# Kernel optimization log

Hardware: AMD Instinct MI355X
Metric: run time of the kernel (lower is better)

## Reference

```python
import jax, jax.numpy as jnp
import numpy as np

DIM = 192
HEADS = 6
WS = 7        # window_size
SS = 3        # shift_size
MLP_RATIO = 4.0
B = 64
H_RES = 56
W_RES = 56
EPS = 1e-5


def _rel_index(ws):
    # standard Swin relative position index, (ws*ws, ws*ws) int
    coords = np.stack(np.meshgrid(np.arange(ws), np.arange(ws), indexing='ij'))  # 2,ws,ws
    flat = coords.reshape(2, -1)                                                 # 2,N
    rel = (flat[:, :, None] - flat[:, None, :]).transpose(1, 2, 0)               # N,N,2
    rel[:, :, 0] += ws - 1
    rel[:, :, 1] += ws - 1
    rel[:, :, 0] *= 2 * ws - 1
    return rel.sum(-1)  # N,N


def _attn_mask(H, W, ws, ss):
    # (num_windows, N, N) float mask with 0 / -100, static given H,W,ws,ss
    img = np.zeros((H, W))
    sl = (slice(0, -ws), slice(-ws, -ss), slice(-ss, None))
    cnt = 0
    for hs in sl:
        for wsl in sl:
            img[hs, wsl] = cnt
            cnt += 1
    mw = img.reshape(H // ws, ws, W // ws, ws).transpose(0, 2, 1, 3).reshape(-1, ws * ws)
    diff = mw[:, None, :] - mw[:, :, None]
    return jnp.asarray(np.where(diff != 0, -100.0, 0.0).astype(np.float32))


def _ln(x, g, b):
    mu = x.mean(-1, keepdims=True)
    var = jnp.var(x, axis=-1, keepdims=True)
    return (x - mu) * jax.lax.rsqrt(var + EPS) * g + b


def setup_inputs() -> dict:
    key = jax.random.key(0)
    ks = jax.random.split(key, 8)
    C = DIM
    hid = int(C * MLP_RATIO)
    nrm = lambda k, s: jax.random.normal(k, s, jnp.float32) * 0.02
    return {
        "x": jax.random.normal(ks[0], (B, H_RES * W_RES, C), jnp.float32),
        "norm1_g": jnp.ones((C,), jnp.float32),
        "norm1_b": jnp.zeros((C,), jnp.float32),
        "qkv_w": nrm(ks[1], (3 * C, C)),
        "qkv_b": jnp.zeros((3 * C,), jnp.float32),
        "rel_bias_table": nrm(ks[2], ((2 * WS - 1) ** 2, HEADS)),
        "proj_w": nrm(ks[3], (C, C)),
        "proj_b": jnp.zeros((C,), jnp.float32),
        "norm2_g": jnp.ones((C,), jnp.float32),
        "norm2_b": jnp.zeros((C,), jnp.float32),
        "fc1_w": nrm(ks[4], (hid, C)),
        "fc1_b": jnp.zeros((hid,), jnp.float32),
        "fc2_w": nrm(ks[5], (C, hid)),
        "fc2_b": jnp.zeros((C,), jnp.float32),
        "H": H_RES,
        "W": W_RES,
    }


def _block(x, norm1_g, norm1_b, qkv_w, qkv_b, rel_bias_table, proj_w, proj_b,
           norm2_g, norm2_b, fc1_w, fc1_b, fc2_w, fc2_b, H, W):
    Bn, L, C = x.shape
    ws = min(WS, H, W)
    ss = SS if ws > SS else 0
    nH, nW = H // ws, W // ws
    N = ws * ws
    hd = C // HEADS

    shortcut = x
    h = _ln(x, norm1_g, norm1_b).reshape(Bn, H, W, C)
    if ss > 0:
        h = jnp.roll(h, (-ss, -ss), axis=(1, 2))
    # window partition -> (Bn*nH*nW, N, C)
    win = h.reshape(Bn, nH, ws, nW, ws, C).transpose(0, 1, 3, 2, 4, 5).reshape(-1, N, C)

    qkv = win @ qkv_w.T + qkv_b                       # (nWin, N, 3C)
    qkv = qkv.reshape(-1, N, 3, HEADS, hd).transpose(2, 0, 3, 1, 4)
    q, k, v = qkv[0], qkv[1], qkv[2]                  # (nWin, heads, N, hd)
    scale = float(hd) ** -0.5
    attn = jnp.einsum('whnd,whmd->whnm', q * scale, k)

    idx = _rel_index(ws)                              # N,N (static)
    bias = rel_bias_table[idx.reshape(-1)].reshape(N, N, HEADS).transpose(2, 0, 1)
    attn = attn + bias[None]

    if ss > 0:
        mask = _attn_mask(H, W, ws, ss)               # (nH*nW, N, N)
        attn = attn.reshape(Bn, nH * nW, HEADS, N, N) + mask[None, :, None]
        attn = attn.reshape(-1, HEADS, N, N)

    attn = jax.nn.softmax(attn, axis=-1)
    out = jnp.einsum('whnm,whmd->whnd', attn, v)      # (nWin, heads, N, hd)
    out = out.transpose(0, 2, 1, 3).reshape(-1, N, C)
    out = out @ proj_w.T + proj_b

    # window reverse -> (Bn, H, W, C)
    out = out.reshape(Bn, nH, nW, ws, ws, C).transpose(0, 1, 3, 2, 4, 5).reshape(Bn, H, W, C)
    if ss > 0:
        out = jnp.roll(out, (ss, ss), axis=(1, 2))
    x = shortcut + out.reshape(Bn, H * W, C)

    h2 = _ln(x, norm2_g, norm2_b)
    h2 = jax.nn.gelu(h2 @ fc1_w.T + fc1_b, approximate=False)
    h2 = h2 @ fc2_w.T + fc2_b
    return x + h2


def reference(x, norm1_g, norm1_b, qkv_w, qkv_b, rel_bias_table, proj_w, proj_b,
              norm2_g, norm2_b, fc1_w, fc1_b, fc2_w, fc2_b, H, W):
    return _block(x, norm1_g, norm1_b, qkv_w, qkv_b, rel_bias_table, proj_w, proj_b,
                  norm2_g, norm2_b, fc1_w, fc1_b, fc2_w, fc2_b, H, W)
```

## Files before the change

### kernel.cpp

```cpp
#include <hip/hip_runtime.h>
#include <math.h>

typedef __attribute__((ext_vector_type(8))) short short8;
typedef __attribute__((ext_vector_type(4))) float floatx4;
typedef __attribute__((ext_vector_type(4))) float fvec4;

__device__ __forceinline__ float bf2f(unsigned short u) {
    union { unsigned int i; float f; } v;
    v.i = ((unsigned int)u) << 16;
    return v.f;
}
__device__ __forceinline__ unsigned short f2bf(float f) {
    union { float f; unsigned int i; } v;
    v.f = f;
    return (unsigned short)((v.i + 0x7FFFu + ((v.i >> 16) & 1u)) >> 16);
}
__device__ __forceinline__ void async16(const void* g, void* l) {
    __builtin_amdgcn_global_load_lds((const __attribute__((address_space(1))) void*)g,
                                     (__attribute__((address_space(3))) void*)l, 16, 0, 0);
}
__device__ __forceinline__ int region(int c) { return c < 49 ? 0 : (c < 53 ? 1 : 2); }

__global__ __launch_bounds__(256) void cvt_kernel(const float* __restrict__ s,
                                                  unsigned short* __restrict__ d, int n) {
    int i = blockIdx.x * 256 + threadIdx.x;
    if (i < n) d[i] = f2bf(s[i]);
}

__global__ __launch_bounds__(256) void ln_kernel(const float* __restrict__ src,
                                                 const float* __restrict__ gw,
                                                 const float* __restrict__ bw,
                                                 unsigned short* __restrict__ dst,
                                                 int mode) {
    int o = blockIdx.x * 4 + (threadIdx.x >> 6);
    int lane = threadIdx.x & 63;
    size_t srow;
    if (mode == 0) {
        int win = o / 49, n = o % 49;
        int b = win >> 6, wl = win & 63;
        int wh = wl >> 3, ww = wl & 7;
        int i = n / 7, j = n % 7;
        int pr = (wh * 7 + i + 3) % 56;
        int pc = (ww * 7 + j + 3) % 56;
        srow = ((size_t)b * 3136 + (size_t)(pr * 56 + pc)) * 192;
    } else {
        srow = (size_t)o * 192;
    }
    float v0 = src[srow + lane];
    float v1 = src[srow + lane + 64];
    float v2 = src[srow + lane + 128];
    float s = v0 + v1 + v2;
    float s2 = v0 * v0 + v1 * v1 + v2 * v2;
    #pragma unroll
    for (int off = 32; off > 0; off >>= 1) {
        s += __shfl_xor(s, off);
        s2 += __shfl_xor(s2, off);
    }
    float mean = s * (1.0f / 192.0f);
    float var = s2 * (1.0f / 192.0f) - mean * mean;
    float inv = rsqrtf(var + 1e-5f);
    size_t drow = (size_t)o * 192;
    dst[drow + lane]       = f2bf((v0 - mean) * inv * gw[lane]       + bw[lane]);
    dst[drow + lane + 64]  = f2bf((v1 - mean) * inv * gw[lane + 64]  + bw[lane + 64]);
    dst[drow + lane + 128] = f2bf((v2 - mean) * inv * gw[lane + 128] + bw[lane + 128]);
}

template <int EPI>
__global__ __launch_bounds__(256) void gemm_nt(const unsigned short* __restrict__ A,
                                               const unsigned short* __restrict__ W,
                                               const float* __restrict__ bias,
                                               int K, int ldo, int mbase,
                                               unsigned short* __restrict__ outb,
                                               float* __restrict__ outf,
                                               const float* __restrict__ resid) {
    __shared__ __align__(16) unsigned short Al[128][32];
    __shared__ __align__(16) unsigned short Wl[64][32];
    int tid = threadIdx.x;
    int lane = tid & 63;
    int wv = tid >> 6;
    int wm = wv >> 1, wn = wv & 1;
    int m0 = blockIdx.y * 128;
    int n0 = blockIdx.x * 64;
    int quad = lane >> 4, l15 = lane & 15;

    int srow = lane >> 2;
    int scol = (lane & 3) * 8;
    const unsigned short* aP0 = A + (size_t)(m0 + wv * 32 + srow) * K + scol;
    const unsigned short* aP1 = aP0 + (size_t)16 * K;
    const unsigned short* wP  = W + (size_t)(n0 + wv * 16 + srow) * K + scol;
    unsigned short* lA0 = &Al[wv * 32][0];
    unsigned short* lA1 = &Al[wv * 32 + 16][0];
    unsigned short* lW  = &Wl[wv * 16][0];

    floatx4 acc[4][2];
    floatx4 zero = {0.f, 0.f, 0.f, 0.f};
    #pragma unroll
    for (int a = 0; a < 4; ++a)
        #pragma unroll
        for (int b = 0; b < 2; ++b) acc[a][b] = zero;

    for (int kt = 0; kt < K; kt += 32) {
        __syncthreads();
        async16(aP0 + kt, lA0);
        async16(aP1 + kt, lA1);
        async16(wP + kt, lW);
        __syncthreads();
        short8 af[4], wf[2];
        #pragma unroll
        for (int mt = 0; mt < 4; ++mt)
            af[mt] = *(const short8*)&Al[wm * 64 + mt * 16 + l15][quad * 8];
        #pragma unroll
        for (int nt = 0; nt < 2; ++nt)
            wf[nt] = *(const short8*)&Wl[wn * 32 + nt * 16 + l15][quad * 8];
        #pragma unroll
        for (int mt = 0; mt < 4; ++mt)
            #pragma unroll
            for (int nt = 0; nt < 2; ++nt)
                acc[mt][nt] = __builtin_amdgcn_mfma_f32_16x16x32_bf16(af[mt], wf[nt], acc[mt][nt], 0, 0, 0);
    }

    #pragma unroll
    for (int mt = 0; mt < 4; ++mt) {
        #pragma unroll
        for (int nt = 0; nt < 2; ++nt) {
            #pragma unroll
            for (int r = 0; r < 4; ++r) {
                int m = m0 + wm * 64 + mt * 16 + quad * 4 + r;
                int n = n0 + wn * 32 + nt * 16 + l15;
                float v = acc[mt][nt][r] + bias[n];
                if (EPI == 0) {
                    outb[(size_t)m * ldo + n] = f2bf(v);
                } else if (EPI == 1) {
                    float g = 0.5f * v * (1.0f + erff(v * 0.70710678118654752f));
                    outb[(size_t)m * ldo + n] = f2bf(g);
                } else if (EPI == 2) {
                    int win = m / 49, np = m % 49;
                    int b = win >> 6, wl = win & 63;
                    int wh = wl >> 3, ww = wl & 7;
                    int i = np / 7, j = np % 7;
                    int pr = (wh * 7 + i + 3) % 56;
                    int pc = (ww * 7 + j + 3) % 56;
                    size_t dst = ((size_t)b * 3136 + (size_t)(pr * 56 + pc)) * 192 + n;
                    outf[dst] = resid[dst] + v;
                } else {
                    size_t dst = (size_t)(mbase + m) * ldo + n;
                    outf[dst] = resid[dst] + v;
                }
            }
        }
    }
}

__global__ __launch_bounds__(192) void attn_kernel(const unsigned short* __restrict__ qkv,
                                                   const float* __restrict__ btab,
                                                   unsigned short* __restrict__ awin) {
    __shared__ __align__(16) unsigned short VT[3][32][72];
    __shared__ __align__(16) unsigned short Pb[3][64][72];
    __shared__ float bl[1014];
    int w = blockIdx.x >> 1;
    int hb = (blockIdx.x & 1) * 3;
    int tid = threadIdx.x;
    int hl = tid >> 6;
    int lane = tid & 63;
    int h = hb + hl;
    int quad = lane >> 4, l15 = lane & 15;
    const unsigned short* base = qkv + (size_t)w * 49 * 576;

    for (int i = tid; i < 1014; i += 192) bl[i] = btab[i];
    for (int idx = lane; idx < 512; idx += 64) {
        VT[hl][idx >> 4][48 + (idx & 15)] = 0;
    }
    for (int idx = lane; idx < 196; idx += 64) {
        int r = idx >> 2, c8 = (idx & 3) * 8;
        short8 vv = *(const short8*)(base + (size_t)r * 576 + 384 + h * 32 + c8);
        #pragma unroll
        for (int e = 0; e < 8; ++e) VT[hl][c8 + e][r] = (unsigned short)vv[e];
    }
    short8 qf[4], kf[4];
    #pragma unroll
    for (int mt = 0; mt < 4; ++mt)
        qf[mt] = *(const short8*)(base + (size_t)(mt * 16 + l15) * 576 + h * 32 + quad * 8);
    #pragma unroll
    for (int nt = 0; nt < 4; ++nt)
        kf[nt] = *(const short8*)(base + (size_t)(nt * 16 + l15) * 576 + 192 + h * 32 + quad * 8);

    floatx4 zero = {0.f, 0.f, 0.f, 0.f};
    floatx4 S[4][4];
    #pragma unroll
    for (int mt = 0; mt < 4; ++mt)
        #pragma unroll
        for (int nt = 0; nt < 4; ++nt)
            S[mt][nt] = __builtin_amdgcn_mfma_f32_16x16x32_bf16(qf[mt], kf[nt], zero, 0, 0, 0);

    __syncthreads();

    int wl = w & 63, wh7 = (wl >> 3) * 7, ww7 = (wl & 7) * 7;
    int coli[4], colj[4], colrid[4], colok[4];
    #pragma unroll
    for (int nt = 0; nt < 4; ++nt) {
        int c = nt * 16 + l15;
        colok[nt] = c < 49;
        int ci = c / 7;
        coli[nt] = ci;
        colj[nt] = c - ci * 7;
        colrid[nt] = region(wh7 + ci) * 3 + region(ww7 + (c - ci * 7));
    }
    const float scale = 0.17677669529663687f;
    float rinv[4][4];
    #pragma unroll
    for (int mt = 0; mt < 4; ++mt) {
        #pragma unroll
        for (int rr = 0; rr < 4; ++rr) {
            int r = mt * 16 + quad * 4 + rr;
            int ri = r / 7, rj = r - ri * 7;
            int rowrid = region(wh7 + ri) * 3 + region(ww7 + rj);
            float vv[4];
            float mx = -3.0e38f;
            #pragma unroll
            for (int nt = 0; nt < 4; ++nt) {
                float v;
                if (colok[nt]) {
                    v = S[mt][nt][rr] * scale +
                        bl[((ri - coli[nt] + 6) * 13 + (rj - colj[nt] + 6)) * 6 + h];
                    if (colrid[nt] != rowrid) v -= 100.f;
                } else {
                    v = -3.0e38f;
                }
                vv[nt] = v;
                mx = fmaxf(mx, v);
            }
            #pragma unroll
            for (int s = 1; s <= 8; s <<= 1) mx = fmaxf(mx, __shfl_xor(mx, s));
            float sum = 0.f;
            #pragma unroll
            for (int nt = 0; nt < 4; ++nt) {
                float e = __expf(vv[nt] - mx);
                vv[nt] = e;
                sum += e;
            }
            #pragma unroll
            for (int s = 1; s <= 8; s <<= 1) sum += __shfl_xor(sum, s);
            rinv[mt][rr] = 1.f / sum;
            #pragma unroll
            for (int nt = 0; nt < 4; ++nt) Pb[hl][r][nt * 16 + l15] = f2bf(vv[nt]);
        }
    }

    floatx4 O[4][2];
    #pragma unroll
    for (int mt = 0; mt < 4; ++mt)
        #pragma unroll
        for (int nt = 0; nt < 2; ++nt) O[mt][nt] = zero;
    #pragma unroll
    for (int ks = 0; ks < 2; ++ks) {
        short8 vf[2];
        #pragma unroll
        for (int nt = 0; nt < 2; ++nt)
            vf[nt] = *(const short8*)&VT[hl][nt * 16 + l15][ks * 32 + quad * 8];
        #pragma unroll
        for (int mt = 0; mt < 4; ++mt) {
            short8 pf = *(const short8*)&Pb[hl][mt * 16 + l15][ks * 32 + quad * 8];
            #pragma unroll
            for (int nt = 0; nt < 2; ++nt)
                O[mt][nt] = __builtin_amdgcn_mfma_f32_16x16x32_bf16(pf, vf[nt], O[mt][nt], 0, 0, 0);
        }
    }
    #pragma unroll
    for (int mt = 0; mt < 4; ++mt) {
        #pragma unroll
        for (int rr = 0; rr < 4; ++rr) {
            int r = mt * 16 + quad * 4 + rr;
            if (r < 49) {
                float inv = rinv[mt][rr];
                #pragma unroll
                for (int nt = 0; nt < 2; ++nt)
                    awin[((size_t)w * 49 + r) * 192 + h * 32 + nt * 16 + l15] =
                        f2bf(O[mt][nt][rr] * inv);
            }
        }
    }
}

extern "C" void kernel_launch(void* const* d_in, const int* in_sizes, int n_in,
                              void* d_out, int out_size, void* d_ws, size_t ws_size,
                              hipStream_t stream) {
    const float* x      = (const float*)d_in[0];
    const float* n1g    = (const float*)d_in[1];
    const float* n1b    = (const float*)d_in[2];
    const float* qkv_w  = (const float*)d_in[3];
    const float* qkv_b  = (const float*)d_in[4];
    const float* btab   = (const float*)d_in[5];
    const float* proj_w = (const float*)d_in[6];
    const float* proj_b = (const float*)d_in[7];
    const float* n2g    = (const float*)d_in[8];
    const float* n2b    = (const float*)d_in[9];
    const float* fc1_w  = (const float*)d_in[10];
    const float* fc1_b  = (const float*)d_in[11];
    const float* fc2_w  = (const float*)d_in[12];
    const float* fc2_b  = (const float*)d_in[13];
    float* out = (float*)d_out;

    char* p = (char*)d_ws;
    size_t off = 0;
    auto alloc = [&](size_t bytes) {
        char* r = p + off;
        off = (off + bytes + 255) & ~(size_t)255;
        return r;
    };
    unsigned short* wq   = (unsigned short*)alloc((size_t)576 * 192 * 2);
    unsigned short* wp   = (unsigned short*)alloc((size_t)192 * 192 * 2);
    unsigned short* w1   = (unsigned short*)alloc((size_t)768 * 192 * 2);
    unsigned short* w2   = (unsigned short*)alloc((size_t)192 * 768 * 2);
    unsigned short* hwin = (unsigned short*)alloc((size_t)200704 * 192 * 2);
    unsigned short* qkvb = (unsigned short*)alloc((size_t)200704 * 576 * 2);
    float*          xres = (float*)alloc((size_t)200704 * 192 * 4);
    unsigned short* g1   = (unsigned short*)alloc((size_t)50176 * 768 * 2);
    if (ws_size < off) return;

    cvt_kernel<<<432, 256, 0, stream>>>(qkv_w, wq, 110592);
    cvt_kernel<<<144, 256, 0, stream>>>(proj_w, wp, 36864);
    cvt_kernel<<<576, 256, 0, stream>>>(fc1_w, w1, 147456);
    cvt_kernel<<<576, 256, 0, stream>>>(fc2_w, w2, 147456);

    ln_kernel<<<50176, 256, 0, stream>>>(x, n1g, n1b, hwin, 0);
    gemm_nt<0><<<dim3(9, 1568), 256, 0, stream>>>(hwin, wq, qkv_b, 192, 576, 0, qkvb, nullptr, nullptr);
    attn_kernel<<<8192, 192, 0, stream>>>(qkvb, btab, hwin );
    gemm_nt<2><<<dim3(3, 1568), 256, 0, stream>>>(hwin, wp, proj_b, 192, 192, 0, nullptr, xres, x);
    unsigned short* h2 = qkvb;
    ln_kernel<<<50176, 256, 0, stream>>>(xres, n2g, n2b, h2, 1);
    for (int c = 0; c < 4; ++c) {
        int mb = c * 50176;
        gemm_nt<1><<<dim3(12, 392), 256, 0, stream>>>(h2 + (size_t)mb * 192, w1, fc1_b, 192, 768, 0,
                                                      g1, nullptr, nullptr);
        gemm_nt<3><<<dim3(3, 392), 256, 0, stream>>>(g1, w2, fc2_b, 768, 192, mb,
                                                     nullptr, out, xres);
    }
}
```

Baseline: 1.133 ms.

## Precompute bias+mask table as MFMA accumulator init and simplify attention softmax

Folds the attention scale into the Q rows of the QKV weights and bias during conversion. A 4-class × heads table of relative bias plus shift mask is precomputed and fed as the MFMA accumulator init. Scores are computed transposed so the per-query sum needs only two cross-lane shuffles. The max subtraction and the LDS transpose of V are dropped, so V is gathered straight from global memory and the block barrier goes away. This removes per-element index math, shared-memory bias loads and sync, at the cost of strided 2-byte V loads and no overflow guard in the exponent.

```diff
diff --git a/kernel.cpp b/kernel.cpp
--- a/kernel.cpp
+++ b/kernel.cpp
@@ -1,9 +1,9 @@
 #include <hip/hip_runtime.h>
+#include <hip/hip_bf16.h>
 #include <math.h>
 
 typedef __attribute__((ext_vector_type(8))) short short8;
 typedef __attribute__((ext_vector_type(4))) float floatx4;
-typedef __attribute__((ext_vector_type(4))) float fvec4;
 
 __device__ __forceinline__ float bf2f(unsigned short u) {
     union { unsigned int i; float f; } v;
@@ -19,12 +19,39 @@
     __builtin_amdgcn_global_load_lds((const __attribute__((address_space(1))) void*)g,
                                      (__attribute__((address_space(3))) void*)l, 16, 0, 0);
 }
-__device__ __forceinline__ int region(int c) { return c < 49 ? 0 : (c < 53 ? 1 : 2); }
 
 __global__ __launch_bounds__(256) void cvt_kernel(const float* __restrict__ s,
-                                                  unsigned short* __restrict__ d, int n) {
+                                                  unsigned short* __restrict__ d, int n,
+                                                  int cut, float scale) {
     int i = blockIdx.x * 256 + threadIdx.x;
-    if (i < n) d[i] = f2bf(s[i]);
+    if (i < n) d[i] = f2bf(s[i] * (i < cut ? scale : 1.0f));
+}
+__global__ __launch_bounds__(256) void biasscale_kernel(const float* __restrict__ s,
+                                                        float* __restrict__ d, int n,
+                                                        int cut, float scale) {
+    int i = blockIdx.x * 256 + threadIdx.x;
+    if (i < n) d[i] = s[i] * (i < cut ? scale : 1.0f);
+}
+
+__global__ __launch_bounds__(256) void bmt_kernel(const float* __restrict__ btab,
+                                                  float* __restrict__ tbl) {
+    int idx = blockIdx.x * 256 + threadIdx.x;
+    int key = idx & 63;
+    int q = (idx >> 6) & 63;
+    int h = (idx >> 12) % 6;
+    int cls = idx / (4096 * 6);
+    float v;
+    if (key >= 49) v = -3.0e38f;
+    else if (q >= 49) v = 0.0f;
+    else {
+        int qi = q / 7, qj = q % 7, ki = key / 7, kj = key % 7;
+        v = btab[((qi - ki + 6) * 13 + (qj - kj + 6)) * 6 + h];
+        int whT = (cls >> 1) & 1, wwT = cls & 1;
+        int rq = (whT ? (qi < 4 ? 1 : 2) : 0) * 3 + (wwT ? (qj < 4 ? 1 : 2) : 0);
+        int rk = (whT ? (ki < 4 ? 1 : 2) : 0) * 3 + (wwT ? (kj < 4 ? 1 : 2) : 0);
+        if (rq != rk) v -= 100.0f;
+    }
+    tbl[idx] = v;
 }
 
 __global__ __launch_bounds__(256) void ln_kernel(const float* __restrict__ src,
@@ -152,101 +179,74 @@
 }
 
 __global__ __launch_bounds__(192) void attn_kernel(const unsigned short* __restrict__ qkv,
-                                                   const float* __restrict__ btab,
+                                                   const float* __restrict__ tbl,
                                                    unsigned short* __restrict__ awin) {
-    __shared__ __align__(16) unsigned short VT[3][32][72];
     __shared__ __align__(16) unsigned short Pb[3][64][72];
-    __shared__ float bl[1014];
     int w = blockIdx.x >> 1;
     int hb = (blockIdx.x & 1) * 3;
-    int tid = threadIdx.x;
-    int hl = tid >> 6;
-    int lane = tid & 63;
+    int hl = threadIdx.x >> 6;
     int h = hb + hl;
+    int lane = threadIdx.x & 63;
     int quad = lane >> 4, l15 = lane & 15;
     const unsigned short* base = qkv + (size_t)w * 49 * 576;
-
-    for (int i = tid; i < 1014; i += 192) bl[i] = btab[i];
-    for (int idx = lane; idx < 512; idx += 64) {
-        VT[hl][idx >> 4][48 + (idx & 15)] = 0;
-    }
-    for (int idx = lane; idx < 196; idx += 64) {
-        int r = idx >> 2, c8 = (idx & 3) * 8;
-        short8 vv = *(const short8*)(base + (size_t)r * 576 + 384 + h * 32 + c8);
-        #pragma unroll
-        for (int e = 0; e < 8; ++e) VT[hl][c8 + e][r] = (unsigned short)vv[e];
-    }
-    short8 qf[4], kf[4];
+    int wl = w & 63;
+    int cls = ((wl >> 3) == 7 ? 2 : 0) + ((wl & 7) == 7 ? 1 : 0);
+    const float* tb = tbl + (size_t)(cls * 6 + h) * 4096;
+
+    short8 kf[4], qf[4];
     #pragma unroll
     for (int mt = 0; mt < 4; ++mt)
-        qf[mt] = *(const short8*)(base + (size_t)(mt * 16 + l15) * 576 + h * 32 + quad * 8);
+        kf[mt] = *(const short8*)(base + (size_t)(mt * 16 + l15) * 576 + 192 + h * 32 + quad * 8);
     #pragma unroll
     for (int nt = 0; nt < 4; ++nt)
-        kf[nt] = *(const short8*)(base + (size_t)(nt * 16 + l15) * 576 + 192 + h * 32 + quad * 8);
-
+        qf[nt] = *(const short8*)(base + (size_t)(nt * 16 + l15) * 576 + h * 32 + quad * 8);
+
+    floatx4 S[4][4];
+    #pragma unroll
+    for (int mt = 0; mt < 4; ++mt)
+        #pragma unroll
+        for (int nt = 0; nt < 4; ++nt) {
+            floatx4 cinit = *(const floatx4*)(tb + (nt * 16 + l15) * 64 + mt * 16 + quad * 4);
+            S[mt][nt] = __builtin_amdgcn_mfma_f32_16x16x32_bf16(kf[mt], qf[nt], cinit, 0, 0, 0);
+        }
+
+    #pragma unroll
+    for (int mt = 0; mt < 4; ++mt)
+        #pragma unroll
+        for (int nt = 0; nt < 4; ++nt)
+            #pragma unroll
+            for (int rr = 0; rr < 4; ++rr)
+                S[mt][nt][rr] = __expf(S[mt][nt][rr]);
+
+    float rinv[4];
+    #pragma unroll
+    for (int nt = 0; nt < 4; ++nt) {
+        float s = 0.f;
+        #pragma unroll
+        for (int mt = 0; mt < 4; ++mt)
+            s += (S[mt][nt][0] + S[mt][nt][1]) + (S[mt][nt][2] + S[mt][nt][3]);
+        s += __shfl_xor(s, 16);
+        s += __shfl_xor(s, 32);
+        rinv[nt] = 1.0f / s;
+    }
+
+    #pragma unroll
+    for (int mt = 0; mt < 4; ++mt) {
+        #pragma unroll
+        for (int nt = 0; nt < 4; ++nt) {
+            __hip_bfloat162 p0 = __float22bfloat162_rn(
+                make_float2(S[mt][nt][0] * rinv[nt], S[mt][nt][1] * rinv[nt]));
+            __hip_bfloat162 p1 = __float22bfloat162_rn(
+                make_float2(S[mt][nt][2] * rinv[nt], S[mt][nt][3] * rinv[nt]));
+            union { __hip_bfloat162 h2[2]; uint2 u; } pk;
+            pk.h2[0] = p0;
+            pk.h2[1] = p1;
+            *(uint2*)&Pb[hl][nt * 16 + l15][mt * 16 + quad * 4] = pk.u;
+        }
+    }
+
+    floatx4 O[4][2];
     floatx4 zero = {0.f, 0.f, 0.f, 0.f};
-    floatx4 S[4][4];
-    #pragma unroll
-    for (int mt = 0; mt < 4; ++mt)
-        #pragma unroll
-        for (int nt = 0; nt < 4; ++nt)
-            S[mt][nt] = __builtin_amdgcn_mfma_f32_16x16x32_bf16(qf[mt], kf[nt], zero, 0, 0, 0);
-
-    __syncthreads();
-
-    int wl = w & 63, wh7 = (wl >> 3) * 7, ww7 = (wl & 7) * 7;
-    int coli[4], colj[4], colrid[4], colok[4];
-    #pragma unroll
-    for (int nt = 0; nt < 4; ++nt) {
-        int c = nt * 16 + l15;
-        colok[nt] = c < 49;
-        int ci = c / 7;
-        coli[nt] = ci;
-        colj[nt] = c - ci * 7;
-        colrid[nt] = region(wh7 + ci) * 3 + region(ww7 + (c - ci * 7));
-    }
-    const float scale = 0.17677669529663687f;
-    float rinv[4][4];
-    #pragma unroll
-    for (int mt = 0; mt < 4; ++mt) {
-        #pragma unroll
-        for (int rr = 0; rr < 4; ++rr) {
-            int r = mt * 16 + quad * 4 + rr;
-            int ri = r / 7, rj = r - ri * 7;
-            int rowrid = region(wh7 + ri) * 3 + region(ww7 + rj);
-            float vv[4];
-            float mx = -3.0e38f;
-            #pragma unroll
-            for (int nt = 0; nt < 4; ++nt) {
-                float v;
-                if (colok[nt]) {
-                    v = S[mt][nt][rr] * scale +
-                        bl[((ri - coli[nt] + 6) * 13 + (rj - colj[nt] + 6)) * 6 + h];
-                    if (colrid[nt] != rowrid) v -= 100.f;
-                } else {
-                    v = -3.0e38f;
-                }
-                vv[nt] = v;
-                mx = fmaxf(mx, v);
-            }
-            #pragma unroll
-            for (int s = 1; s <= 8; s <<= 1) mx = fmaxf(mx, __shfl_xor(mx, s));
-            float sum = 0.f;
-            #pragma unroll
-            for (int nt = 0; nt < 4; ++nt) {
-                float e = __expf(vv[nt] - mx);
-                vv[nt] = e;
-                sum += e;
-            }
-            #pragma unroll
-            for (int s = 1; s <= 8; s <<= 1) sum += __shfl_xor(sum, s);
-            rinv[mt][rr] = 1.f / sum;
-            #pragma unroll
-            for (int nt = 0; nt < 4; ++nt) Pb[hl][r][nt * 16 + l15] = f2bf(vv[nt]);
-        }
-    }
-
-    floatx4 O[4][2];
     #pragma unroll
     for (int mt = 0; mt < 4; ++mt)
         #pragma unroll
@@ -255,8 +255,12 @@
     for (int ks = 0; ks < 2; ++ks) {
         short8 vf[2];
         #pragma unroll
-        for (int nt = 0; nt < 2; ++nt)
-            vf[nt] = *(const short8*)&VT[hl][nt * 16 + l15][ks * 32 + quad * 8];
+        for (int nt = 0; nt < 2; ++nt) {
+            const unsigned short* vb =
+                base + (size_t)(ks * 32 + quad * 8) * 576 + 384 + h * 32 + nt * 16 + l15;
+            #pragma unroll
+            for (int j = 0; j < 8; ++j) vf[nt][j] = (short)vb[(size_t)j * 576];
+        }
         #pragma unroll
         for (int mt = 0; mt < 4; ++mt) {
             short8 pf = *(const short8*)&Pb[hl][mt * 16 + l15][ks * 32 + quad * 8];
@@ -269,13 +273,12 @@
     for (int mt = 0; mt < 4; ++mt) {
         #pragma unroll
         for (int rr = 0; rr < 4; ++rr) {
-            int r = mt * 16 + quad * 4 + rr;
-            if (r < 49) {
-                float inv = rinv[mt][rr];
+            int q = mt * 16 + quad * 4 + rr;
+            if (q < 49) {
                 #pragma unroll
                 for (int nt = 0; nt < 2; ++nt)
-                    awin[((size_t)w * 49 + r) * 192 + h * 32 + nt * 16 + l15] =
-                        f2bf(O[mt][nt][rr] * inv);
+                    awin[((size_t)w * 49 + q) * 192 + h * 32 + nt * 16 + l15] =
+                        f2bf(O[mt][nt][rr]);
             }
         }
     }
@@ -316,15 +319,20 @@
     float*          xres = (float*)alloc((size_t)200704 * 192 * 4);
     unsigned short* g1   = (unsigned short*)alloc((size_t)50176 * 768 * 2);
     if (ws_size < off) return;
-
-    cvt_kernel<<<432, 256, 0, stream>>>(qkv_w, wq, 110592);
-    cvt_kernel<<<144, 256, 0, stream>>>(proj_w, wp, 36864);
-    cvt_kernel<<<576, 256, 0, stream>>>(fc1_w, w1, 147456);
-    cvt_kernel<<<576, 256, 0, stream>>>(fc2_w, w2, 147456);
+    float* tbl   = (float*)g1;
+    float* qkvbs = (float*)g1 + 98304;
+
+    const float scale = 0.17677669529663687f;
+    cvt_kernel<<<432, 256, 0, stream>>>(qkv_w, wq, 110592, 36864, scale);
+    cvt_kernel<<<144, 256, 0, stream>>>(proj_w, wp, 36864, 0, 1.0f);
+    cvt_kernel<<<576, 256, 0, stream>>>(fc1_w, w1, 147456, 0, 1.0f);
+    cvt_kernel<<<576, 256, 0, stream>>>(fc2_w, w2, 147456, 0, 1.0f);
+    biasscale_kernel<<<3, 256, 0, stream>>>(qkv_b, qkvbs, 576, 192, scale);
+    bmt_kernel<<<384, 256, 0, stream>>>(btab, tbl);
 
     ln_kernel<<<50176, 256, 0, stream>>>(x, n1g, n1b, hwin, 0);
-    gemm_nt<0><<<dim3(9, 1568), 256, 0, stream>>>(hwin, wq, qkv_b, 192, 576, 0, qkvb, nullptr, nullptr);
-    attn_kernel<<<8192, 192, 0, stream>>>(qkvb, btab, hwin );
+    gemm_nt<0><<<dim3(9, 1568), 256, 0, stream>>>(hwin, wq, qkvbs, 192, 576, 0, qkvb, nullptr, nullptr);
+    attn_kernel<<<8192, 192, 0, stream>>>(qkvb, tbl, hwin );
     gemm_nt<2><<<dim3(3, 1568), 256, 0, stream>>>(hwin, wp, proj_b, 192, 192, 0, nullptr, xres, x);
     unsigned short* h2 = qkvb;
     ln_kernel<<<50176, 256, 0, stream>>>(xres, n2g, n2b, h2, 1);
```

Result: faster. 1.101 ms (-2.8%).
